# Kernel optimization log

Hardware: AMD Instinct MI355X
Metric: run time of the kernel (lower is better)

Reference implementation:

```python
import jax, jax.numpy as jnp
import numpy as np

H = 64
VOCAB = 64
THRESH_SCALE = 0.4
LN_EPS = 1e-5
NORM_EPS = 1e-12


def setup_inputs() -> dict:
    key = jax.random.key(0)
    ks = jax.random.split(key, 16)
    B, L = 64, 1024
    s = 1.0 / np.sqrt(H)
    inp = {
        "seq": jax.random.randint(ks[0], (B, L), 0, VOCAB),
        "embed_W": jax.random.normal(ks[1], (VOCAB, H), jnp.float32),
        "ff_W1": jax.random.normal(ks[2], (H, 2 * H), jnp.float32) * s,
        "ff_b1": jnp.zeros((2 * H,), jnp.float32),
        "ff_W2": jax.random.normal(ks[3], (2 * H, H), jnp.float32) * s,
        "ff_b2": jnp.zeros((H,), jnp.float32),
        "ln_g": jnp.ones((H,), jnp.float32),
        "ln_b": jnp.zeros((H,), jnp.float32),
        "kp_W": jax.random.normal(ks[4], (H, H), jnp.float32) * s,
        "vp_W": jax.random.normal(ks[5], (H, H), jnp.float32) * s,
        "qp_W": jax.random.normal(ks[6], (H, H), jnp.float32) * s,
        "rp_W": jax.random.normal(ks[7], (H, H), jnp.float32) * s,
        "rp_b": jnp.zeros((H,), jnp.float32),
        "out_W": jax.random.normal(ks[8], (H, VOCAB), jnp.float32) * s,
        "out_b": jnp.zeros((VOCAB,), jnp.float32),
    }
    return inp


def _forward(seq, embed_W, ff_W1, ff_b1, ff_W2, ff_b2, ln_g, ln_b,
             kp_W, vp_W, qp_W, rp_W, rp_b, out_W, out_b):
    h = embed_W[seq]                                    # [B, L, H]
    ff = jnp.maximum(h @ ff_W1 + ff_b1, 0.0) @ ff_W2 + ff_b2
    x = h + ff
    mu = x.mean(-1, keepdims=True)
    var = ((x - mu) ** 2).mean(-1, keepdims=True)       # biased var (torch LayerNorm)
    hn = (x - mu) / jnp.sqrt(var + LN_EPS) * ln_g + ln_b
    B, L, _ = hn.shape

    # Precompute all per-step keys/values, then scan the fast-weight update.
    k_all = hn[:, :-1] @ kp_W                           # [B, L-1, H]
    v_all = hn[:, :-1] @ vp_W                           # [B, L-1, H]
    kn_all = k_all / jnp.maximum(
        jnp.linalg.norm(k_all, axis=-1, keepdims=True), NORM_EPS)

    def step(M, kv):
        kn, v = kv                                      # each [B, H]
        vp = jnp.einsum('bij,bj->bi', M, kn)            # read M along k
        err = jnp.linalg.norm(v - vp, axis=-1)          # [B]
        gate = jnp.where(err > THRESH_SCALE * jnp.linalg.norm(v, axis=-1),
                         1.0, 0.0)                      # hard energy gate
        M = M + gate[:, None, None] * jnp.einsum('bi,bj->bij', v - vp, kn)
        return M, None

    M0 = jnp.zeros((B, H, H), dtype=hn.dtype)
    M, _ = jax.lax.scan(step, M0,
                        (kn_all.transpose(1, 0, 2), v_all.transpose(1, 0, 2)))

    q = hn[:, -1] @ qp_W                                # [B, H]
    r = jnp.einsum('bij,bj->bi', M, q) @ rp_W + rp_b
    return r @ out_W + out_b                            # [B, VOCAB]


def reference(seq, embed_W, ff_W1, ff_b1, ff_W2, ff_b2, ln_g, ln_b,
              kp_W, vp_W, qp_W, rp_W, rp_b, out_W, out_b):
    return _forward(seq, embed_W, ff_W1, ff_b1, ff_W2, ff_b2, ln_g, ln_b,
                    kp_W, vp_W, qp_W, rp_W, rp_b, out_W, out_b)
```

## Files before the change

kernel.cpp:

```cpp
#include <hip/hip_runtime.h>
#include <hip/hip_bf16.h>
#include <math.h>

#define BB 64
#define LL 1024
#define HH 64

typedef float v4f __attribute__((ext_vector_type(4)));
#define F4 __builtin_elementwise_fma

__global__ __launch_bounds__(256, 1)
void token_kernel(const int* __restrict__ seq,
                  const float* __restrict__ embed_W,
                  const float* __restrict__ ff_W1, const float* __restrict__ ff_b1,
                  const float* __restrict__ ff_W2, const float* __restrict__ ff_b2,
                  const float* __restrict__ ln_g, const float* __restrict__ ln_b,
                  const float* __restrict__ kp_W, const float* __restrict__ vp_W,
                  const float* __restrict__ qp_W,
                  float* __restrict__ knv, float* __restrict__ vthr,
                  float* __restrict__ qbuf)
{
    __shared__ __align__(16) float h_s[32][64];
    __shared__ __align__(16) float t1_s[32][128];
    __shared__ __align__(16) float hn_s[32][64];

    const int tid  = threadIdx.x;
    const int tok0 = blockIdx.x * 32;

#pragma unroll
    for (int k = 0; k < 8; ++k) {
        int e   = k * 256 + tid;
        int tok = e >> 6, i = e & 63;
        int s   = seq[tok0 + tok];
        h_s[tok][i] = embed_W[s * 64 + i];
    }
    __syncthreads();

    {
        const int j = tid & 127;
        const int g = tid >> 7;
        float w1c[64];
#pragma unroll
        for (int ii = 0; ii < 64; ++ii) w1c[ii] = ff_W1[ii * 128 + j];
        const float b1j = ff_b1[j];
#pragma unroll
        for (int tk = 0; tk < 16; ++tk) {
            const int tok = g * 16 + tk;
            const float4* h4 = (const float4*)h_s[tok];
            float a0 = b1j, a1 = 0.f, a2 = 0.f, a3 = 0.f;
#pragma unroll
            for (int w = 0; w < 16; ++w) {
                float4 hv = h4[w];
                a0 = fmaf(hv.x, w1c[4*w+0], a0);
                a1 = fmaf(hv.y, w1c[4*w+1], a1);
                a2 = fmaf(hv.z, w1c[4*w+2], a2);
                a3 = fmaf(hv.w, w1c[4*w+3], a3);
            }
            t1_s[tok][j] = fmaxf((a0 + a1) + (a2 + a3), 0.f);
        }
    }
    __syncthreads();

    {
        const int i  = tid & 63;
        const int w4 = tid >> 6;
        const float b2i = ff_b2[i];
        const float gi  = ln_g[i];
        const float bi  = ln_b[i];
        float accf[8];
#pragma unroll
        for (int tk = 0; tk < 8; ++tk) accf[tk] = b2i;
#pragma unroll
        for (int h = 0; h < 2; ++h) {
            float w2c[64];
#pragma unroll
            for (int jj = 0; jj < 64; ++jj) w2c[jj] = ff_W2[(h*64 + jj) * 64 + i];
#pragma unroll
            for (int tk = 0; tk < 8; ++tk) {
                const int tok = w4 * 8 + tk;
                const float4* t4 = (const float4*)&t1_s[tok][h*64];
                float a0 = 0.f, a1 = 0.f, a2 = 0.f, a3 = 0.f;
#pragma unroll
                for (int w = 0; w < 16; ++w) {
                    float4 tv = t4[w];
                    a0 = fmaf(tv.x, w2c[4*w+0], a0);
                    a1 = fmaf(tv.y, w2c[4*w+1], a1);
                    a2 = fmaf(tv.z, w2c[4*w+2], a2);
                    a3 = fmaf(tv.w, w2c[4*w+3], a3);
                }
                accf[tk] += (a0 + a1) + (a2 + a3);
            }
        }
#pragma unroll
        for (int tk = 0; tk < 8; ++tk) {
            const int tok = w4 * 8 + tk;
            float x = h_s[tok][i] + accf[tk];
            float s = x;
#pragma unroll
            for (int m = 32; m > 0; m >>= 1) s += __shfl_xor(s, m);
            float mu = s * (1.f / 64.f);
            float d  = x - mu;
            float s2 = d * d;
#pragma unroll
            for (int m = 32; m > 0; m >>= 1) s2 += __shfl_xor(s2, m);
            float var = s2 * (1.f / 64.f);
            hn_s[tok][i] = d / sqrtf(var + 1e-5f) * gi + bi;
        }
    }
    __syncthreads();

    {
        const int i  = tid & 63;
        const int w4 = tid >> 6;
        float kc[64], vc[64];
#pragma unroll
        for (int ii = 0; ii < 64; ++ii) {
            kc[ii] = kp_W[ii * 64 + i];
            vc[ii] = vp_W[ii * 64 + i];
        }
#pragma unroll
        for (int tk = 0; tk < 8; ++tk) {
            const int tok = w4 * 8 + tk;
            const int tg  = tok0 + tok;
            const int b   = tg >> 10;
            const int t   = tg & 1023;
            const float4* hn4 = (const float4*)hn_s[tok];
            if (t < 1023) {
                float ka0=0.f,ka1=0.f,ka2=0.f,ka3=0.f;
                float va0=0.f,va1=0.f,va2=0.f,va3=0.f;
#pragma unroll
                for (int w = 0; w < 16; ++w) {
                    float4 hv = hn4[w];
                    ka0 = fmaf(hv.x, kc[4*w+0], ka0);
                    ka1 = fmaf(hv.y, kc[4*w+1], ka1);
                    ka2 = fmaf(hv.z, kc[4*w+2], ka2);
                    ka3 = fmaf(hv.w, kc[4*w+3], ka3);
                    va0 = fmaf(hv.x, vc[4*w+0], va0);
                    va1 = fmaf(hv.y, vc[4*w+1], va1);
                    va2 = fmaf(hv.z, vc[4*w+2], va2);
                    va3 = fmaf(hv.w, vc[4*w+3], va3);
                }
                float ka = (ka0 + ka1) + (ka2 + ka3);
                float va = (va0 + va1) + (va2 + va3);
                float kn2 = ka * ka, vn2 = va * va;
#pragma unroll
                for (int m = 32; m > 0; m >>= 1) {
                    kn2 += __shfl_xor(kn2, m);
                    vn2 += __shfl_xor(vn2, m);
                }
                float knorm = fmaxf(sqrtf(kn2), 1e-12f);
                size_t row = ((size_t)b * 1024 + t) * 128;
                knv[row + i]      = ka / knorm;
                knv[row + 64 + i] = va;
                if (i == 0) vthr[b * 1024 + t] = 0.16f * vn2;
            } else {
                float qa0=0.f,qa1=0.f,qa2=0.f,qa3=0.f;
#pragma unroll
                for (int w = 0; w < 16; ++w) {
                    float4 hv = hn4[w];
                    qa0 = fmaf(hv.x, qp_W[(4*w+0)*64 + i], qa0);
                    qa1 = fmaf(hv.y, qp_W[(4*w+1)*64 + i], qa1);
                    qa2 = fmaf(hv.z, qp_W[(4*w+2)*64 + i], qa2);
                    qa3 = fmaf(hv.w, qp_W[(4*w+3)*64 + i], qa3);
                }
                qbuf[b * 64 + i] = (qa0 + qa1) + (qa2 + qa3);
            }
        }
    }
}


template<int CTRL>
__device__ __forceinline__ float dppadd(float x) {
    int y = __builtin_amdgcn_update_dpp(0, __float_as_int(x), CTRL, 0xF, 0xF, true);
    return x + __int_as_float(y);
}

__device__ __forceinline__ float bcast63(float x) {
    return __int_as_float(__builtin_amdgcn_readlane(__float_as_int(x), 63));
}

__device__ __forceinline__ float wave_sum64(float x) {
    x = dppadd<0x111>(x); x = dppadd<0x112>(x);
    x = dppadd<0x114>(x); x = dppadd<0x118>(x);
    x = dppadd<0x142>(x); x = dppadd<0x143>(x);
    return bcast63(x);
}

__device__ __forceinline__ void wsum4(float& a, float& b, float& c, float& d) {
    a = dppadd<0x111>(a); b = dppadd<0x111>(b); c = dppadd<0x111>(c); d = dppadd<0x111>(d);
    a = dppadd<0x112>(a); b = dppadd<0x112>(b); c = dppadd<0x112>(c); d = dppadd<0x112>(d);
    a = dppadd<0x114>(a); b = dppadd<0x114>(b); c = dppadd<0x114>(c); d = dppadd<0x114>(d);
    a = dppadd<0x118>(a); b = dppadd<0x118>(b); c = dppadd<0x118>(c); d = dppadd<0x118>(d);
    a = dppadd<0x142>(a); b = dppadd<0x142>(b); c = dppadd<0x142>(c); d = dppadd<0x142>(d);
    a = dppadd<0x143>(a); b = dppadd<0x143>(b); c = dppadd<0x143>(c); d = dppadd<0x143>(d);
    a = bcast63(a); b = bcast63(b); c = bcast63(c); d = bcast63(d);
}

#define LOADK4(P, ROW) do { \
    const float* r_ = (ROW) + (wid << 4); \
    P##0 = *(const v4f*)(r_ + 0);  P##1 = *(const v4f*)(r_ + 4); \
    P##2 = *(const v4f*)(r_ + 8);  P##3 = *(const v4f*)(r_ + 12); \
} while (0)

#define UPD4(P, G) do { \
    v4f gv_ = {G, G, G, G}; \
    m0 = F4(gv_, P##0, m0); m1 = F4(gv_, P##1, m1); \
    m2 = F4(gv_, P##2, m2); m3 = F4(gv_, P##3, m3); \
} while (0)

#define CHUNK2(UP, UQ, XR, XS, ROW2, ROW3, TH2P, TH3P, PAR) do { \
    UPD4(UP, gdp); \
    UPD4(UQ, gdq); \
    v4f q_ = F4(m0, XR##0, F4(m1, XR##1, F4(m2, XR##2, m3 * XR##3))); \
    float own0_ = (q_.x + q_.y) + (q_.z + q_.w); \
    v4f r_ = F4(m0, XS##0, F4(m1, XS##1, F4(m2, XS##2, m3 * XS##3))); \
    float own1_ = (r_.x + r_.y) + (r_.z + r_.w); \
    ((float2*)pex[PAR][wid])[lane] = make_float2(own0_, own1_); \
    asm volatile("s_waitcnt lgkmcnt(0)\n\ts_barrier" ::: "memory"); \
    float2 p0_ = ((const float2*)pex[PAR][0])[lane]; \
    float2 p1_ = ((const float2*)pex[PAR][1])[lane]; \
    float2 p2_ = ((const float2*)pex[PAR][2])[lane]; \
    float2 p3_ = ((const float2*)pex[PAR][3])[lane]; \
    float knl2_ = (ROW2)[lane]; \
    float knl3_ = (ROW3)[lane]; \
    float vv2_  = (ROW2)[64 + lane]; \
    float vv3_  = (ROW3)[64 + lane]; \
    float th2_  = *(TH2P); \
    float th3_  = *(TH3P); \
    LOADK4(UP, ROW2); \
    LOADK4(UQ, ROW3); \
    float base0_ = (p0_.x + p1_.x) + (p2_.x + p3_.x); \
    float base1_ = (p0_.y + p1_.y) + (p2_.y + p3_.y); \
    float d00_ = vv0 - base0_; \
    float d01_ = vv1 - base1_; \
    float x0_ = d00_ * d00_, x1_ = d00_ * d01_; \
    float x2_ = d01_ * d01_, x3_ = knl2_ * knl3_; \
    wsum4(x0_, x1_, x2_, x3_); \
    bool g0_ = x0_ > th0; \
    float corr_ = fmaf(2.f * c3, x1_, -(c3 * c3) * x0_); \
    float e1_ = g0_ ? (x2_ - corr_) : x2_; \
    bool g1_ = e1_ > th1; \
    float gd0_ = g0_ ? d00_ : 0.f; \
    float d1_  = fmaf(-c3, gd0_, d01_); \
    gdp = gd0_; \
    gdq = g1_ ? d1_ : 0.f; \
    vv0 = vv2_; vv1 = vv3_; th0 = th2_; th1 = th3_; c3 = x3_; \
} while (0)

#define BUF8(CB, NB, TP) \
    CHUNK2(U,V,S,T,(CB)+2*128, (CB)+3*128, (TP)+2, (TP)+3, 0); \
    CHUNK2(S,T,U,V,(CB)+4*128, (CB)+5*128, (TP)+4, (TP)+5, 1); \
    CHUNK2(U,V,S,T,(CB)+6*128, (CB)+7*128, (TP)+6, (TP)+7, 0); \
    CHUNK2(S,T,U,V,(CB)+8*128, (CB)+9*128, (TP)+8, (TP)+9, 1); \
    CHUNK2(U,V,S,T,(CB)+10*128,(CB)+11*128,(TP)+10,(TP)+11,0); \
    CHUNK2(S,T,U,V,(CB)+12*128,(CB)+13*128,(TP)+12,(TP)+13,1); \
    CHUNK2(U,V,S,T,(CB)+14*128,(CB)+15*128,(TP)+14,(TP)+15,0); \
    CHUNK2(S,T,U,V,(NB)+0*128, (NB)+1*128, (TP)+16,(TP)+17,1);

__device__ __forceinline__ void gl2lds_1k(const float* g, float* l, int lane) {
    __builtin_amdgcn_global_load_lds(
        (const __attribute__((address_space(1))) void*)(g + lane * 4),
        (__attribute__((address_space(3))) void*)l, 16, 0, 0);
}

__device__ __forceinline__ void prefetch_quarter(const float* g, float* l,
                                                 int lane, int wid) {
#pragma unroll
    for (int j = 0; j < 2; ++j)
        gl2lds_1k(g + wid * 512 + j * 256, l + wid * 512 + j * 256, lane);
}

__global__ __launch_bounds__(256, 1)
void scan_kernel(const float* __restrict__ knv,
                 const float* __restrict__ vthr,
                 const float* __restrict__ qbuf,
                 const float* __restrict__ rp_W, const float* __restrict__ rp_b,
                 const float* __restrict__ out_W, const float* __restrict__ out_b,
                 float* __restrict__ out)
{
    const int b    = blockIdx.x;
    const int tid  = threadIdx.x;
    const int lane = tid & 63;
    const int wid  = tid >> 6;
    const float* knvb = knv  + (size_t)b * 1024 * 128;
    const float* thrb = vthr + (size_t)b * 1024;

    __shared__ __align__(16) float thr_s[1040];
    __shared__ __align__(16) float buf[3 * 2048];
    __shared__ __align__(16) float pex[2][4][128];
    __shared__ float sh[64];

    v4f m0={0,0,0,0}, m1={0,0,0,0}, m2={0,0,0,0}, m3={0,0,0,0};
    v4f S0,S1,S2,S3;
    v4f T0,T1,T2,T3;
    v4f U0,U1,U2,U3;
    v4f V0,V1,V2,V3;

    if (wid == 0) {
#pragma unroll
        for (int w = 0; w < 4; ++w) gl2lds_1k(thrb + w * 256, thr_s + w * 256, lane);
    }
    prefetch_quarter(knvb,        buf,        lane, wid);
    prefetch_quarter(knvb + 2048, buf + 2048, lane, wid);
    prefetch_quarter(knvb + 4096, buf + 4096, lane, wid);

    {
        float4 z4 = make_float4(0.f, 0.f, 0.f, 0.f);
        ((float4*)pex)[tid] = z4;
    }

    asm volatile("s_waitcnt vmcnt(2) lgkmcnt(0)\n\ts_barrier" ::: "memory");

    LOADK4(S, buf);
    LOADK4(T, buf + 128);
    {
        v4f z_ = {0.f, 0.f, 0.f, 0.f};
        U0=z_;U1=z_;U2=z_;U3=z_;
        V0=z_;V1=z_;V2=z_;V3=z_;
    }
    float vv0 = buf[64 + lane];
    float vv1 = buf[192 + lane];
    float th0 = thr_s[0];
    float th1 = thr_s[1];
    float c3  = wave_sum64(buf[lane] * buf[128 + lane]);
    float gdp = 0.f, gdq = 0.f;

#pragma unroll 1
    for (int c = 0; c < 62; ++c) {
        asm volatile("s_waitcnt vmcnt(2)" ::: "memory");
        const float* cb = buf + (c % 3) * 2048;
        const float* nb = buf + ((c + 1) % 3) * 2048;
        const float* tp = thr_s + c * 16;
        BUF8(cb, nb, tp)
        if (c <= 60)
            prefetch_quarter(knvb + (size_t)(c + 3) * 2048,
                             buf + (c % 3) * 2048, lane, wid);
    }
    asm volatile("s_waitcnt vmcnt(0)" ::: "memory");
    asm volatile("s_barrier" ::: "memory");
    {
        const float* cb = buf + 2 * 2048;
        const float* nb = buf;
        const float* tp = thr_s + 62 * 16;
        BUF8(cb, nb, tp)
    }
    {
        const float* cb = buf;
        const float* nb = buf + 2048;
        const float* tp = thr_s + 63 * 16;
        BUF8(cb, nb, tp)
    }
    UPD4(U, gdp);

    {
        const v4f* qq = (const v4f*)(qbuf + b * 64);
        const int w4i = 4 * wid;
        v4f aq = F4(m0, qq[w4i+0], F4(m1, qq[w4i+1],
                 F4(m2, qq[w4i+2],  m3 * qq[w4i+3])));
        float vq_own = (aq.x + aq.y) + (aq.z + aq.w);
        pex[0][wid][lane] = vq_own;
        asm volatile("s_waitcnt lgkmcnt(0)\n\ts_barrier" ::: "memory");

        if (wid == 0) {
            float vq = (pex[0][0][lane] + pex[0][1][lane])
                     + (pex[0][2][lane] + pex[0][3][lane]);
            sh[lane] = vq;
            asm volatile("s_waitcnt lgkmcnt(0)" ::: "memory");
            float r = rp_b[lane];
#pragma unroll
            for (int ii = 0; ii < 64; ++ii) r = fmaf(sh[ii], rp_W[ii * 64 + lane], r);
            asm volatile("s_waitcnt lgkmcnt(0)" ::: "memory");
            sh[lane] = r;
            asm volatile("s_waitcnt lgkmcnt(0)" ::: "memory");
            float o = out_b[lane];
#pragma unroll
            for (int ii = 0; ii < 64; ++ii) o = fmaf(sh[ii], out_W[ii * 64 + lane], o);
            out[b * 64 + lane] = o;
        }
    }
}

extern "C" void kernel_launch(void* const* d_in, const int* in_sizes, int n_in,
                              void* d_out, int out_size, void* d_ws, size_t ws_size,
                              hipStream_t stream)
{
    const int*   seq   = (const int*)  d_in[0];
    const float* embed = (const float*)d_in[1];
    const float* ffW1  = (const float*)d_in[2];
    const float* ffb1  = (const float*)d_in[3];
    const float* ffW2  = (const float*)d_in[4];
    const float* ffb2  = (const float*)d_in[5];
    const float* lng   = (const float*)d_in[6];
    const float* lnb   = (const float*)d_in[7];
    const float* kpW   = (const float*)d_in[8];
    const float* vpW   = (const float*)d_in[9];
    const float* qpW   = (const float*)d_in[10];
    const float* rpW   = (const float*)d_in[11];
    const float* rpb   = (const float*)d_in[12];
    const float* outW  = (const float*)d_in[13];
    const float* outb  = (const float*)d_in[14];
    float* out = (float*)d_out;

    float* knv  = (float*)d_ws;
    float* vthr = knv  + (size_t)64 * 1024 * 128;
    float* qbuf = vthr + (size_t)64 * 1024;

    token_kernel<<<2048, 256, 0, stream>>>(seq, embed, ffW1, ffb1, ffW2, ffb2,
                                           lng, lnb, kpW, vpW, qpW,
                                           knv, vthr, qbuf);
    scan_kernel<<<64, 256, 0, stream>>>(knv, vthr, qbuf,
                                        rpW, rpb, outW, outb, out);
}
```

Baseline: 366.1 us.

## Process four scan steps per barrier using pairwise key dot-product corrections

The sequential fast-weight scan now handles four timesteps per cross-wave exchange instead of two. It reads M·k for four future keys at once, then applies gated rank-1 corrections using precomputed pairwise key dot products (six wave reductions per stage). This halves the number of block barriers and LDS exchange rounds along the serial dependency chain. In exchange it adds more register pressure (32 v4f key registers), extra DPP reductions and more serial scalar correction math.

Measured after the change: 348.8 us. 4.7% less time.

```diff
diff --git a/kernel.cpp b/kernel.cpp
--- a/kernel.cpp
+++ b/kernel.cpp
@@ -180,21 +180,14 @@
     return __int_as_float(__builtin_amdgcn_readlane(__float_as_int(x), 63));
 }
 
-__device__ __forceinline__ float wave_sum64(float x) {
-    x = dppadd<0x111>(x); x = dppadd<0x112>(x);
-    x = dppadd<0x114>(x); x = dppadd<0x118>(x);
-    x = dppadd<0x142>(x); x = dppadd<0x143>(x);
-    return bcast63(x);
-}
-
-__device__ __forceinline__ void wsum4(float& a, float& b, float& c, float& d) {
-    a = dppadd<0x111>(a); b = dppadd<0x111>(b); c = dppadd<0x111>(c); d = dppadd<0x111>(d);
-    a = dppadd<0x112>(a); b = dppadd<0x112>(b); c = dppadd<0x112>(c); d = dppadd<0x112>(d);
-    a = dppadd<0x114>(a); b = dppadd<0x114>(b); c = dppadd<0x114>(c); d = dppadd<0x114>(d);
-    a = dppadd<0x118>(a); b = dppadd<0x118>(b); c = dppadd<0x118>(c); d = dppadd<0x118>(d);
-    a = dppadd<0x142>(a); b = dppadd<0x142>(b); c = dppadd<0x142>(c); d = dppadd<0x142>(d);
-    a = dppadd<0x143>(a); b = dppadd<0x143>(b); c = dppadd<0x143>(c); d = dppadd<0x143>(d);
-    a = bcast63(a); b = bcast63(b); c = bcast63(c); d = bcast63(d);
+__device__ __forceinline__ void wsum6(float& a, float& b, float& c,
+                                      float& d, float& e, float& f) {
+#define LVL(C) a=dppadd<C>(a); b=dppadd<C>(b); c=dppadd<C>(c); \
+               d=dppadd<C>(d); e=dppadd<C>(e); f=dppadd<C>(f);
+    LVL(0x111) LVL(0x112) LVL(0x114) LVL(0x118) LVL(0x142) LVL(0x143)
+#undef LVL
+    a=bcast63(a); b=bcast63(b); c=bcast63(c);
+    d=bcast63(d); e=bcast63(e); f=bcast63(f);
 }
 
 #define LOADK4(P, ROW) do { \
@@ -209,54 +202,69 @@
     m2 = F4(gv_, P##2, m2); m3 = F4(gv_, P##3, m3); \
 } while (0)
 
-#define CHUNK2(UP, UQ, XR, XS, ROW2, ROW3, TH2P, TH3P, PAR) do { \
-    UPD4(UP, gdp); \
-    UPD4(UQ, gdq); \
-    v4f q_ = F4(m0, XR##0, F4(m1, XR##1, F4(m2, XR##2, m3 * XR##3))); \
-    float own0_ = (q_.x + q_.y) + (q_.z + q_.w); \
-    v4f r_ = F4(m0, XS##0, F4(m1, XS##1, F4(m2, XS##2, m3 * XS##3))); \
-    float own1_ = (r_.x + r_.y) + (r_.z + r_.w); \
-    ((float2*)pex[PAR][wid])[lane] = make_float2(own0_, own1_); \
+#define DOT4(P, OUT) do { \
+    v4f t_ = F4(m0, P##0, F4(m1, P##1, F4(m2, P##2, m3 * P##3))); \
+    OUT = (t_.x + t_.y) + (t_.z + t_.w); \
+} while (0)
+
+#define CHUNK4(U0_, U1_, U2_, U3_, D0_, D1_, D2_, D3_, R4, R5, R6, R7, \
+               T4, T5, T6, T7, PAR) do { \
+    UPD4(U0_, gd0); UPD4(U1_, gd1); UPD4(U2_, gd2); UPD4(U3_, gd3); \
+    float o0_, o1_, o2_, o3_; \
+    DOT4(D0_, o0_); DOT4(D1_, o1_); DOT4(D2_, o2_); DOT4(D3_, o3_); \
+    ((float4*)pex[PAR][wid])[lane] = make_float4(o0_, o1_, o2_, o3_); \
     asm volatile("s_waitcnt lgkmcnt(0)\n\ts_barrier" ::: "memory"); \
-    float2 p0_ = ((const float2*)pex[PAR][0])[lane]; \
-    float2 p1_ = ((const float2*)pex[PAR][1])[lane]; \
-    float2 p2_ = ((const float2*)pex[PAR][2])[lane]; \
-    float2 p3_ = ((const float2*)pex[PAR][3])[lane]; \
-    float knl2_ = (ROW2)[lane]; \
-    float knl3_ = (ROW3)[lane]; \
-    float vv2_  = (ROW2)[64 + lane]; \
-    float vv3_  = (ROW3)[64 + lane]; \
-    float th2_  = *(TH2P); \
-    float th3_  = *(TH3P); \
-    LOADK4(UP, ROW2); \
-    LOADK4(UQ, ROW3); \
-    float base0_ = (p0_.x + p1_.x) + (p2_.x + p3_.x); \
-    float base1_ = (p0_.y + p1_.y) + (p2_.y + p3_.y); \
-    float d00_ = vv0 - base0_; \
-    float d01_ = vv1 - base1_; \
-    float x0_ = d00_ * d00_, x1_ = d00_ * d01_; \
-    float x2_ = d01_ * d01_, x3_ = knl2_ * knl3_; \
-    wsum4(x0_, x1_, x2_, x3_); \
+    float4 p0_ = ((const float4*)pex[PAR][0])[lane]; \
+    float4 p1_ = ((const float4*)pex[PAR][1])[lane]; \
+    float4 p2_ = ((const float4*)pex[PAR][2])[lane]; \
+    float4 p3_ = ((const float4*)pex[PAR][3])[lane]; \
+    float kn4_ = (R4)[lane], kn5_ = (R5)[lane]; \
+    float kn6_ = (R6)[lane], kn7_ = (R7)[lane]; \
+    float vv4_ = (R4)[64 + lane], vv5_ = (R5)[64 + lane]; \
+    float vv6_ = (R6)[64 + lane], vv7_ = (R7)[64 + lane]; \
+    float t4_ = *(T4), t5_ = *(T5), t6_ = *(T6), t7_ = *(T7); \
+    LOADK4(U0_, R4); LOADK4(U1_, R5); LOADK4(U2_, R6); LOADK4(U3_, R7); \
+    float b0_ = (p0_.x + p1_.x) + (p2_.x + p3_.x); \
+    float b1_ = (p0_.y + p1_.y) + (p2_.y + p3_.y); \
+    float b2_ = (p0_.z + p1_.z) + (p2_.z + p3_.z); \
+    float b3_ = (p0_.w + p1_.w) + (p2_.w + p3_.w); \
+    float d0_ = vv0 - b0_, d1_ = vv1 - b1_; \
+    float d2_ = vv2 - b2_, d3_ = vv3 - b3_; \
+    float x0_ = d0_ * d0_, x1_ = d0_ * d1_, x2_ = d1_ * d1_; \
+    float x3_ = kn4_ * kn5_, x4_ = kn4_ * kn6_, x5_ = kn4_ * kn7_; \
+    wsum6(x0_, x1_, x2_, x3_, x4_, x5_); \
     bool g0_ = x0_ > th0; \
-    float corr_ = fmaf(2.f * c3, x1_, -(c3 * c3) * x0_); \
-    float e1_ = g0_ ? (x2_ - corr_) : x2_; \
+    float co1_ = fmaf(2.f * c01, x1_, -(c01 * c01) * x0_); \
+    float e1_ = g0_ ? (x2_ - co1_) : x2_; \
     bool g1_ = e1_ > th1; \
-    float gd0_ = g0_ ? d00_ : 0.f; \
-    float d1_  = fmaf(-c3, gd0_, d01_); \
-    gdp = gd0_; \
-    gdq = g1_ ? d1_ : 0.f; \
-    vv0 = vv2_; vv1 = vv3_; th0 = th2_; th1 = th3_; c3 = x3_; \
+    float gda_ = g0_ ? d0_ : 0.f; \
+    float gdb_ = g1_ ? fmaf(-c01, gda_, d1_) : 0.f; \
+    float d2p_ = fmaf(-c12, gdb_, fmaf(-c02, gda_, d2_)); \
+    float d3p_ = fmaf(-c13, gdb_, fmaf(-c03, gda_, d3_)); \
+    float y0_ = d2p_ * d2p_, y1_ = d2p_ * d3p_, y2_ = d3p_ * d3p_; \
+    float y3_ = kn5_ * kn6_, y4_ = kn5_ * kn7_, y5_ = kn6_ * kn7_; \
+    wsum6(y0_, y1_, y2_, y3_, y4_, y5_); \
+    bool g2_ = y0_ > th2; \
+    float co2_ = fmaf(2.f * c23, y1_, -(c23 * c23) * y0_); \
+    float e3_ = g2_ ? (y2_ - co2_) : y2_; \
+    bool g3_ = e3_ > th3; \
+    float gdc_ = g2_ ? d2p_ : 0.f; \
+    float gdd_ = g3_ ? fmaf(-c23, gdc_, d3p_) : 0.f; \
+    gd0 = gda_; gd1 = gdb_; gd2 = gdc_; gd3 = gdd_; \
+    c01 = x3_; c02 = x4_; c03 = x5_; c12 = y3_; c13 = y4_; c23 = y5_; \
+    vv0 = vv4_; vv1 = vv5_; vv2 = vv6_; vv3 = vv7_; \
+    th0 = t4_; th1 = t5_; th2 = t6_; th3 = t7_; \
 } while (0)
 
-#define BUF8(CB, NB, TP) \
-    CHUNK2(U,V,S,T,(CB)+2*128, (CB)+3*128, (TP)+2, (TP)+3, 0); \
-    CHUNK2(S,T,U,V,(CB)+4*128, (CB)+5*128, (TP)+4, (TP)+5, 1); \
-    CHUNK2(U,V,S,T,(CB)+6*128, (CB)+7*128, (TP)+6, (TP)+7, 0); \
-    CHUNK2(S,T,U,V,(CB)+8*128, (CB)+9*128, (TP)+8, (TP)+9, 1); \
-    CHUNK2(U,V,S,T,(CB)+10*128,(CB)+11*128,(TP)+10,(TP)+11,0); \
-    CHUNK2(S,T,U,V,(CB)+12*128,(CB)+13*128,(TP)+12,(TP)+13,1); \
-    CHUNK2(U,V,S,T,(CB)+14*128,(CB)+15*128,(TP)+14,(TP)+15,0); \
-    CHUNK2(S,T,U,V,(NB)+0*128, (NB)+1*128, (TP)+16,(TP)+17,1);
+#define BUF4(CB, NB, TP) \
+    CHUNK4(B0,B1,B2,B3, A0,A1,A2,A3, (CB)+4*128,(CB)+5*128,(CB)+6*128,(CB)+7*128, \
+           (TP)+4,(TP)+5,(TP)+6,(TP)+7, 0); \
+    CHUNK4(A0,A1,A2,A3, B0,B1,B2,B3, (CB)+8*128,(CB)+9*128,(CB)+10*128,(CB)+11*128, \
+           (TP)+8,(TP)+9,(TP)+10,(TP)+11, 1); \
+    CHUNK4(B0,B1,B2,B3, A0,A1,A2,A3, (CB)+12*128,(CB)+13*128,(CB)+14*128,(CB)+15*128, \
+           (TP)+12,(TP)+13,(TP)+14,(TP)+15, 0); \
+    CHUNK4(A0,A1,A2,A3, B0,B1,B2,B3, (NB)+0*128,(NB)+1*128,(NB)+2*128,(NB)+3*128, \
+           (TP)+16,(TP)+17,(TP)+18,(TP)+19, 1);
 
 __device__ __forceinline__ void gl2lds_1k(const float* g, float* l, int lane) {
     __builtin_amdgcn_global_load_lds(
@@ -288,14 +296,12 @@
 
     __shared__ __align__(16) float thr_s[1040];
     __shared__ __align__(16) float buf[3 * 2048];
-    __shared__ __align__(16) float pex[2][4][128];
+    __shared__ __align__(16) float pex[2][4][256];
     __shared__ float sh[64];
 
     v4f m0={0,0,0,0}, m1={0,0,0,0}, m2={0,0,0,0}, m3={0,0,0,0};
-    v4f S0,S1,S2,S3;
-    v4f T0,T1,T2,T3;
-    v4f U0,U1,U2,U3;
-    v4f V0,V1,V2,V3;
+    v4f A00,A01,A02,A03, A10,A11,A12,A13, A20,A21,A22,A23, A30,A31,A32,A33;
+    v4f B00,B01,B02,B03, B10,B11,B12,B13, B20,B21,B22,B23, B30,B31,B32,B33;
 
     if (wid == 0) {
 #pragma unroll
@@ -305,26 +311,27 @@
     prefetch_quarter(knvb + 2048, buf + 2048, lane, wid);
     prefetch_quarter(knvb + 4096, buf + 4096, lane, wid);
 
-    {
-        float4 z4 = make_float4(0.f, 0.f, 0.f, 0.f);
-        ((float4*)pex)[tid] = z4;
-    }
-
     asm volatile("s_waitcnt vmcnt(2) lgkmcnt(0)\n\ts_barrier" ::: "memory");
 
-    LOADK4(S, buf);
-    LOADK4(T, buf + 128);
+    LOADK4(A0, buf + 0*128); LOADK4(A1, buf + 1*128);
+    LOADK4(A2, buf + 2*128); LOADK4(A3, buf + 3*128);
     {
         v4f z_ = {0.f, 0.f, 0.f, 0.f};
-        U0=z_;U1=z_;U2=z_;U3=z_;
-        V0=z_;V1=z_;V2=z_;V3=z_;
-    }
-    float vv0 = buf[64 + lane];
-    float vv1 = buf[192 + lane];
-    float th0 = thr_s[0];
-    float th1 = thr_s[1];
-    float c3  = wave_sum64(buf[lane] * buf[128 + lane]);
-    float gdp = 0.f, gdq = 0.f;
+        B00=z_;B01=z_;B02=z_;B03=z_; B10=z_;B11=z_;B12=z_;B13=z_;
+        B20=z_;B21=z_;B22=z_;B23=z_; B30=z_;B31=z_;B32=z_;B33=z_;
+    }
+    float vv0 = buf[0*128+64+lane], vv1 = buf[1*128+64+lane];
+    float vv2 = buf[2*128+64+lane], vv3 = buf[3*128+64+lane];
+    float th0 = thr_s[0], th1 = thr_s[1], th2 = thr_s[2], th3 = thr_s[3];
+    float c01, c02, c03, c12, c13, c23;
+    {
+        float k0_ = buf[0*128+lane], k1_ = buf[1*128+lane];
+        float k2_ = buf[2*128+lane], k3_ = buf[3*128+lane];
+        c01 = k0_*k1_; c02 = k0_*k2_; c03 = k0_*k3_;
+        c12 = k1_*k2_; c13 = k1_*k3_; c23 = k2_*k3_;
+        wsum6(c01, c02, c03, c12, c13, c23);
+    }
+    float gd0 = 0.f, gd1 = 0.f, gd2 = 0.f, gd3 = 0.f;
 
 #pragma unroll 1
     for (int c = 0; c < 62; ++c) {
@@ -332,7 +339,7 @@
         const float* cb = buf + (c % 3) * 2048;
         const float* nb = buf + ((c + 1) % 3) * 2048;
         const float* tp = thr_s + c * 16;
-        BUF8(cb, nb, tp)
+        BUF4(cb, nb, tp)
         if (c <= 60)
             prefetch_quarter(knvb + (size_t)(c + 3) * 2048,
                              buf + (c % 3) * 2048, lane, wid);
@@ -343,15 +350,15 @@
         const float* cb = buf + 2 * 2048;
         const float* nb = buf;
         const float* tp = thr_s + 62 * 16;
-        BUF8(cb, nb, tp)
+        BUF4(cb, nb, tp)
     }
     {
         const float* cb = buf;
         const float* nb = buf + 2048;
         const float* tp = thr_s + 63 * 16;
-        BUF8(cb, nb, tp)
-    }
-    UPD4(U, gdp);
+        BUF4(cb, nb, tp)
+    }
+    UPD4(B0, gd0); UPD4(B1, gd1); UPD4(B2, gd2);
 
     {
         const v4f* qq = (const v4f*)(qbuf + b * 64);
```

## Register-tile token_kernel matmuls to reuse shared-memory activation loads

Applied to the files above, without the earlier changes.

Restructures the FF1, FF2 and K/V projection matmuls in token_kernel into register tiles. Each thread now computes 2 output columns by 4–8 tokens and streams weight rows in chunks of 4, replacing the old scheme of caching a full 64-entry weight column per thread. Each float4 read of activations from shared memory is reused across more FMAs, and the large per-thread weight arrays go away. Cost is extra syncs and a staging pass of FF and K/V results through shared memory before LayerNorm and normalization. The scan kernel, which likely dominates total time, is unchanged.

After: 374.7 us. 1.02x slower.

```diff
diff --git a/kernel.cpp b/kernel.cpp
--- a/kernel.cpp
+++ b/kernel.cpp
@@ -37,26 +37,95 @@
     __syncthreads();
 
     {
-        const int j = tid & 127;
-        const int g = tid >> 7;
-        float w1c[64];
-#pragma unroll
-        for (int ii = 0; ii < 64; ++ii) w1c[ii] = ff_W1[ii * 128 + j];
-        const float b1j = ff_b1[j];
-#pragma unroll
-        for (int tk = 0; tk < 16; ++tk) {
-            const int tok = g * 16 + tk;
-            const float4* h4 = (const float4*)h_s[tok];
-            float a0 = b1j, a1 = 0.f, a2 = 0.f, a3 = 0.f;
-#pragma unroll
-            for (int w = 0; w < 16; ++w) {
-                float4 hv = h4[w];
-                a0 = fmaf(hv.x, w1c[4*w+0], a0);
-                a1 = fmaf(hv.y, w1c[4*w+1], a1);
-                a2 = fmaf(hv.z, w1c[4*w+2], a2);
-                a3 = fmaf(hv.w, w1c[4*w+3], a3);
-            }
-            t1_s[tok][j] = fmaxf((a0 + a1) + (a2 + a3), 0.f);
+        const int jj = tid & 63;
+        const int tg = tid >> 6;
+        float a[2][8][4];
+        const float b10 = ff_b1[jj];
+        const float b11 = ff_b1[jj + 64];
+#pragma unroll
+        for (int t = 0; t < 8; ++t) {
+            a[0][t][0] = b10; a[0][t][1] = 0.f; a[0][t][2] = 0.f; a[0][t][3] = 0.f;
+            a[1][t][0] = b11; a[1][t][1] = 0.f; a[1][t][2] = 0.f; a[1][t][3] = 0.f;
+        }
+#pragma unroll
+        for (int cc = 0; cc < 16; ++cc) {
+            float w0[4], w1[4];
+#pragma unroll
+            for (int r = 0; r < 4; ++r) {
+                w0[r] = ff_W1[(4*cc + r) * 128 + jj];
+                w1[r] = ff_W1[(4*cc + r) * 128 + jj + 64];
+            }
+#pragma unroll
+            for (int t = 0; t < 8; ++t) {
+                const float4 hv = ((const float4*)h_s[tg * 8 + t])[cc];
+                a[0][t][0] = fmaf(hv.x, w0[0], a[0][t][0]);
+                a[0][t][1] = fmaf(hv.y, w0[1], a[0][t][1]);
+                a[0][t][2] = fmaf(hv.z, w0[2], a[0][t][2]);
+                a[0][t][3] = fmaf(hv.w, w0[3], a[0][t][3]);
+                a[1][t][0] = fmaf(hv.x, w1[0], a[1][t][0]);
+                a[1][t][1] = fmaf(hv.y, w1[1], a[1][t][1]);
+                a[1][t][2] = fmaf(hv.z, w1[2], a[1][t][2]);
+                a[1][t][3] = fmaf(hv.w, w1[3], a[1][t][3]);
+            }
+        }
+#pragma unroll
+        for (int t = 0; t < 8; ++t) {
+            const int tok = tg * 8 + t;
+            t1_s[tok][jj]      = fmaxf((a[0][t][0] + a[0][t][1])
+                                     + (a[0][t][2] + a[0][t][3]), 0.f);
+            t1_s[tok][jj + 64] = fmaxf((a[1][t][0] + a[1][t][1])
+                                     + (a[1][t][2] + a[1][t][3]), 0.f);
+        }
+    }
+    __syncthreads();
+
+    {
+        const int ii = tid & 31;
+        const int tg = tid >> 5;
+        const int i0 = ii, i1 = ii + 32;
+        float accf[2][4];
+        const float b20 = ff_b2[i0], b21 = ff_b2[i1];
+#pragma unroll
+        for (int t = 0; t < 4; ++t) { accf[0][t] = b20; accf[1][t] = b21; }
+#pragma unroll
+        for (int h = 0; h < 2; ++h) {
+            float a[2][4][4];
+#pragma unroll
+            for (int t = 0; t < 4; ++t)
+#pragma unroll
+                for (int r = 0; r < 4; ++r) { a[0][t][r] = 0.f; a[1][t][r] = 0.f; }
+#pragma unroll
+            for (int cc = 0; cc < 16; ++cc) {
+                float w0[4], w1[4];
+#pragma unroll
+                for (int r = 0; r < 4; ++r) {
+                    w0[r] = ff_W2[(h*64 + 4*cc + r) * 64 + i0];
+                    w1[r] = ff_W2[(h*64 + 4*cc + r) * 64 + i1];
+                }
+#pragma unroll
+                for (int t = 0; t < 4; ++t) {
+                    const float4 tv = ((const float4*)&t1_s[tg * 4 + t][h * 64])[cc];
+                    a[0][t][0] = fmaf(tv.x, w0[0], a[0][t][0]);
+                    a[0][t][1] = fmaf(tv.y, w0[1], a[0][t][1]);
+                    a[0][t][2] = fmaf(tv.z, w0[2], a[0][t][2]);
+                    a[0][t][3] = fmaf(tv.w, w0[3], a[0][t][3]);
+                    a[1][t][0] = fmaf(tv.x, w1[0], a[1][t][0]);
+                    a[1][t][1] = fmaf(tv.y, w1[1], a[1][t][1]);
+                    a[1][t][2] = fmaf(tv.z, w1[2], a[1][t][2]);
+                    a[1][t][3] = fmaf(tv.w, w1[3], a[1][t][3]);
+                }
+            }
+#pragma unroll
+            for (int t = 0; t < 4; ++t) {
+                accf[0][t] += (a[0][t][0] + a[0][t][1]) + (a[0][t][2] + a[0][t][3]);
+                accf[1][t] += (a[1][t][0] + a[1][t][1]) + (a[1][t][2] + a[1][t][3]);
+            }
+        }
+#pragma unroll
+        for (int t = 0; t < 4; ++t) {
+            const int tok = tg * 4 + t;
+            hn_s[tok][i0] = h_s[tok][i0] + accf[0][t];
+            hn_s[tok][i1] = h_s[tok][i1] + accf[1][t];
         }
     }
     __syncthreads();
@@ -64,37 +133,12 @@
     {
         const int i  = tid & 63;
         const int w4 = tid >> 6;
-        const float b2i = ff_b2[i];
-        const float gi  = ln_g[i];
-        const float bi  = ln_b[i];
-        float accf[8];
-#pragma unroll
-        for (int tk = 0; tk < 8; ++tk) accf[tk] = b2i;
-#pragma unroll
-        for (int h = 0; h < 2; ++h) {
-            float w2c[64];
-#pragma unroll
-            for (int jj = 0; jj < 64; ++jj) w2c[jj] = ff_W2[(h*64 + jj) * 64 + i];
-#pragma unroll
-            for (int tk = 0; tk < 8; ++tk) {
-                const int tok = w4 * 8 + tk;
-                const float4* t4 = (const float4*)&t1_s[tok][h*64];
-                float a0 = 0.f, a1 = 0.f, a2 = 0.f, a3 = 0.f;
-#pragma unroll
-                for (int w = 0; w < 16; ++w) {
-                    float4 tv = t4[w];
-                    a0 = fmaf(tv.x, w2c[4*w+0], a0);
-                    a1 = fmaf(tv.y, w2c[4*w+1], a1);
-                    a2 = fmaf(tv.z, w2c[4*w+2], a2);
-                    a3 = fmaf(tv.w, w2c[4*w+3], a3);
-                }
-                accf[tk] += (a0 + a1) + (a2 + a3);
-            }
-        }
+        const float gi = ln_g[i];
+        const float bi = ln_b[i];
 #pragma unroll
         for (int tk = 0; tk < 8; ++tk) {
             const int tok = w4 * 8 + tk;
-            float x = h_s[tok][i] + accf[tk];
+            float x = hn_s[tok][i];
             float s = x;
 #pragma unroll
             for (int m = 32; m > 0; m >>= 1) s += __shfl_xor(s, m);
@@ -110,38 +154,71 @@
     __syncthreads();
 
     {
+        const int ii = tid & 31;
+        const int tg = tid >> 5;
+        const int i0 = ii, i1 = ii + 32;
+        float ak[2][4][4], av[2][4][4];
+#pragma unroll
+        for (int t = 0; t < 4; ++t)
+#pragma unroll
+            for (int r = 0; r < 4; ++r) {
+                ak[0][t][r] = 0.f; ak[1][t][r] = 0.f;
+                av[0][t][r] = 0.f; av[1][t][r] = 0.f;
+            }
+#pragma unroll
+        for (int cc = 0; cc < 16; ++cc) {
+            float wk0[4], wk1[4], wv0[4], wv1[4];
+#pragma unroll
+            for (int r = 0; r < 4; ++r) {
+                wk0[r] = kp_W[(4*cc + r) * 64 + i0];
+                wk1[r] = kp_W[(4*cc + r) * 64 + i1];
+                wv0[r] = vp_W[(4*cc + r) * 64 + i0];
+                wv1[r] = vp_W[(4*cc + r) * 64 + i1];
+            }
+#pragma unroll
+            for (int t = 0; t < 4; ++t) {
+                const float4 hv = ((const float4*)hn_s[tg * 4 + t])[cc];
+                ak[0][t][0] = fmaf(hv.x, wk0[0], ak[0][t][0]);
+                ak[0][t][1] = fmaf(hv.y, wk0[1], ak[0][t][1]);
+                ak[0][t][2] = fmaf(hv.z, wk0[2], ak[0][t][2]);
+                ak[0][t][3] = fmaf(hv.w, wk0[3], ak[0][t][3]);
+                ak[1][t][0] = fmaf(hv.x, wk1[0], ak[1][t][0]);
+                ak[1][t][1] = fmaf(hv.y, wk1[1], ak[1][t][1]);
+                ak[1][t][2] = fmaf(hv.z, wk1[2], ak[1][t][2]);
+                ak[1][t][3] = fmaf(hv.w, wk1[3], ak[1][t][3]);
+                av[0][t][0] = fmaf(hv.x, wv0[0], av[0][t][0]);
+                av[0][t][1] = fmaf(hv.y, wv0[1], av[0][t][1]);
+                av[0][t][2] = fmaf(hv.z, wv0[2], av[0][t][2]);
+                av[0][t][3] = fmaf(hv.w, wv0[3], av[0][t][3]);
+                av[1][t][0] = fmaf(hv.x, wv1[0], av[1][t][0]);
+                av[1][t][1] = fmaf(hv.y, wv1[1], av[1][t][1]);
+                av[1][t][2] = fmaf(hv.z, wv1[2], av[1][t][2]);
+                av[1][t][3] = fmaf(hv.w, wv1[3], av[1][t][3]);
+            }
+        }
+#pragma unroll
+        for (int t = 0; t < 4; ++t) {
+            const int tok = tg * 4 + t;
+            t1_s[tok][i0]      = (ak[0][t][0] + ak[0][t][1]) + (ak[0][t][2] + ak[0][t][3]);
+            t1_s[tok][i1]      = (ak[1][t][0] + ak[1][t][1]) + (ak[1][t][2] + ak[1][t][3]);
+            t1_s[tok][64 + i0] = (av[0][t][0] + av[0][t][1]) + (av[0][t][2] + av[0][t][3]);
+            t1_s[tok][64 + i1] = (av[1][t][0] + av[1][t][1]) + (av[1][t][2] + av[1][t][3]);
+        }
+    }
+    __syncthreads();
+
+    {
         const int i  = tid & 63;
         const int w4 = tid >> 6;
-        float kc[64], vc[64];
-#pragma unroll
-        for (int ii = 0; ii < 64; ++ii) {
-            kc[ii] = kp_W[ii * 64 + i];
-            vc[ii] = vp_W[ii * 64 + i];
-        }
 #pragma unroll
         for (int tk = 0; tk < 8; ++tk) {
             const int tok = w4 * 8 + tk;
-            const int tg  = tok0 + tok;
-            const int b   = tg >> 10;
-            const int t   = tg & 1023;
-            const float4* hn4 = (const float4*)hn_s[tok];
+            const int tg_ = tok0 + tok;
+            const int b   = tg_ >> 10;
+            const int t   = tg_ & 1023;
             if (t < 1023) {
-                float ka0=0.f,ka1=0.f,ka2=0.f,ka3=0.f;
-                float va0=0.f,va1=0.f,va2=0.f,va3=0.f;
-#pragma unroll
-                for (int w = 0; w < 16; ++w) {
-                    float4 hv = hn4[w];
-                    ka0 = fmaf(hv.x, kc[4*w+0], ka0);
-                    ka1 = fmaf(hv.y, kc[4*w+1], ka1);
-                    ka2 = fmaf(hv.z, kc[4*w+2], ka2);
-                    ka3 = fmaf(hv.w, kc[4*w+3], ka3);
-                    va0 = fmaf(hv.x, vc[4*w+0], va0);
-                    va1 = fmaf(hv.y, vc[4*w+1], va1);
-                    va2 = fmaf(hv.z, vc[4*w+2], va2);
-                    va3 = fmaf(hv.w, vc[4*w+3], va3);
-                }
-                float ka = (ka0 + ka1) + (ka2 + ka3);
-                float va = (va0 + va1) + (va2 + va3);
+                float ka = t1_s[tok][i];
+                float va = t1_s[tok][64 + i];
                 float kn2 = ka * ka, vn2 = va * va;
 #pragma unroll
                 for (int m = 32; m > 0; m >>= 1) {
@@ -154,6 +231,7 @@
                 knv[row + 64 + i] = va;
                 if (i == 0) vthr[b * 1024 + t] = 0.16f * vn2;
             } else {
+                const float4* hn4 = (const float4*)hn_s[tok];
                 float qa0=0.f,qa1=0.f,qa2=0.f,qa3=0.f;
 #pragma unroll
                 for (int w = 0; w < 16; ++w) {
```

## Software-pipeline scan readout one step ahead using Gram-matrix corrections

Applied to the files above, without the earlier changes.

Restructures the sequential fast-weight scan so each step computes the M·k readout for the next pair before the pending rank-1 update is applied. The missing contribution is added back through precomputed key dot products (Ga/Gb terms). The cross-wave exchange barrier now sits at the end of the step, so it overlaps with the next step's loads and updates and shortens the serial dependency chain. In exchange, each step adds more DPP reductions (8 instead of 4) and extra FMAs, and the corrected readout may differ slightly in floating-point results from the direct form.

Result: slower. 395.7 us (+8.1%).

```diff
diff --git a/kernel.cpp b/kernel.cpp
--- a/kernel.cpp
+++ b/kernel.cpp
@@ -187,14 +187,14 @@
     return bcast63(x);
 }
 
-__device__ __forceinline__ void wsum4(float& a, float& b, float& c, float& d) {
-    a = dppadd<0x111>(a); b = dppadd<0x111>(b); c = dppadd<0x111>(c); d = dppadd<0x111>(d);
-    a = dppadd<0x112>(a); b = dppadd<0x112>(b); c = dppadd<0x112>(c); d = dppadd<0x112>(d);
-    a = dppadd<0x114>(a); b = dppadd<0x114>(b); c = dppadd<0x114>(c); d = dppadd<0x114>(d);
-    a = dppadd<0x118>(a); b = dppadd<0x118>(b); c = dppadd<0x118>(c); d = dppadd<0x118>(d);
-    a = dppadd<0x142>(a); b = dppadd<0x142>(b); c = dppadd<0x142>(c); d = dppadd<0x142>(d);
-    a = dppadd<0x143>(a); b = dppadd<0x143>(b); c = dppadd<0x143>(c); d = dppadd<0x143>(d);
-    a = bcast63(a); b = bcast63(b); c = bcast63(c); d = bcast63(d);
+__device__ __forceinline__ void wsum8(float& a, float& b, float& c, float& d,
+                                      float& e, float& f, float& g, float& h) {
+#define LVL(C) a=dppadd<C>(a); b=dppadd<C>(b); c=dppadd<C>(c); d=dppadd<C>(d); \
+               e=dppadd<C>(e); f=dppadd<C>(f); g=dppadd<C>(g); h=dppadd<C>(h);
+    LVL(0x111) LVL(0x112) LVL(0x114) LVL(0x118) LVL(0x142) LVL(0x143)
+#undef LVL
+    a=bcast63(a); b=bcast63(b); c=bcast63(c); d=bcast63(d);
+    e=bcast63(e); f=bcast63(f); g=bcast63(g); h=bcast63(h);
 }
 
 #define LOADK4(P, ROW) do { \
@@ -209,54 +209,58 @@
     m2 = F4(gv_, P##2, m2); m3 = F4(gv_, P##3, m3); \
 } while (0)
 
-#define CHUNK2(UP, UQ, XR, XS, ROW2, ROW3, TH2P, TH3P, PAR) do { \
-    UPD4(UP, gdp); \
-    UPD4(UQ, gdq); \
-    v4f q_ = F4(m0, XR##0, F4(m1, XR##1, F4(m2, XR##2, m3 * XR##3))); \
-    float own0_ = (q_.x + q_.y) + (q_.z + q_.w); \
-    v4f r_ = F4(m0, XS##0, F4(m1, XS##1, F4(m2, XS##2, m3 * XS##3))); \
-    float own1_ = (r_.x + r_.y) + (r_.z + r_.w); \
-    ((float2*)pex[PAR][wid])[lane] = make_float2(own0_, own1_); \
-    asm volatile("s_waitcnt lgkmcnt(0)\n\ts_barrier" ::: "memory"); \
-    float2 p0_ = ((const float2*)pex[PAR][0])[lane]; \
-    float2 p1_ = ((const float2*)pex[PAR][1])[lane]; \
-    float2 p2_ = ((const float2*)pex[PAR][2])[lane]; \
-    float2 p3_ = ((const float2*)pex[PAR][3])[lane]; \
+#define CHUNK2L(P0_, P1_, ROW2, ROW3, TH2P, TH3P, PAR) do { \
+    float2 p0_ = ((const float2*)pex[(PAR)^1][0])[lane]; \
+    float2 p1_ = ((const float2*)pex[(PAR)^1][1])[lane]; \
+    float2 p2_ = ((const float2*)pex[(PAR)^1][2])[lane]; \
+    float2 p3_ = ((const float2*)pex[(PAR)^1][3])[lane]; \
+    UPD4(P0_, gdp); \
+    UPD4(P1_, gdq); \
+    LOADK4(P0_, ROW2); \
+    LOADK4(P1_, ROW3); \
     float knl2_ = (ROW2)[lane]; \
     float knl3_ = (ROW3)[lane]; \
     float vv2_  = (ROW2)[64 + lane]; \
     float vv3_  = (ROW3)[64 + lane]; \
     float th2_  = *(TH2P); \
     float th3_  = *(TH3P); \
-    LOADK4(UP, ROW2); \
-    LOADK4(UQ, ROW3); \
     float base0_ = (p0_.x + p1_.x) + (p2_.x + p3_.x); \
     float base1_ = (p0_.y + p1_.y) + (p2_.y + p3_.y); \
-    float d00_ = vv0 - base0_; \
-    float d01_ = vv1 - base1_; \
-    float x0_ = d00_ * d00_, x1_ = d00_ * d01_; \
-    float x2_ = d01_ * d01_, x3_ = knl2_ * knl3_; \
-    wsum4(x0_, x1_, x2_, x3_); \
+    float vp0_ = fmaf(Gb0, gdq, fmaf(Ga0, gdp, base0_)); \
+    float vp1_ = fmaf(Gb1, gdq, fmaf(Ga1, gdp, base1_)); \
+    float d00_ = vv0 - vp0_; \
+    float d01_ = vv1 - vp1_; \
+    float x0_ = d00_ * d00_, x1_ = d00_ * d01_, x2_ = d01_ * d01_; \
+    float y0_ = knl0 * knl2_, y1_ = knl1 * knl2_; \
+    float y2_ = knl0 * knl3_, y3_ = knl1 * knl3_, y4_ = knl2_ * knl3_; \
+    wsum8(x0_, x1_, x2_, y0_, y1_, y2_, y3_, y4_); \
     bool g0_ = x0_ > th0; \
-    float corr_ = fmaf(2.f * c3, x1_, -(c3 * c3) * x0_); \
+    float corr_ = fmaf(2.f * c01, x1_, -(c01 * c01) * x0_); \
     float e1_ = g0_ ? (x2_ - corr_) : x2_; \
     bool g1_ = e1_ > th1; \
     float gd0_ = g0_ ? d00_ : 0.f; \
-    float d1_  = fmaf(-c3, gd0_, d01_); \
+    float d1_  = fmaf(-c01, gd0_, d01_); \
     gdp = gd0_; \
     gdq = g1_ ? d1_ : 0.f; \
-    vv0 = vv2_; vv1 = vv3_; th0 = th2_; th1 = th3_; c3 = x3_; \
+    v4f q_ = F4(m0, P0_##0, F4(m1, P0_##1, F4(m2, P0_##2, m3 * P0_##3))); \
+    float own0_ = (q_.x + q_.y) + (q_.z + q_.w); \
+    v4f r_ = F4(m0, P1_##0, F4(m1, P1_##1, F4(m2, P1_##2, m3 * P1_##3))); \
+    float own1_ = (r_.x + r_.y) + (r_.z + r_.w); \
+    ((float2*)pex[PAR][wid])[lane] = make_float2(own0_, own1_); \
+    knl0 = knl2_; knl1 = knl3_; vv0 = vv2_; vv1 = vv3_; th0 = th2_; th1 = th3_; \
+    Ga0 = y0_; Gb0 = y1_; Ga1 = y2_; Gb1 = y3_; c01 = y4_; \
+    asm volatile("s_waitcnt lgkmcnt(0)\n\ts_barrier" ::: "memory"); \
 } while (0)
 
-#define BUF8(CB, NB, TP) \
-    CHUNK2(U,V,S,T,(CB)+2*128, (CB)+3*128, (TP)+2, (TP)+3, 0); \
-    CHUNK2(S,T,U,V,(CB)+4*128, (CB)+5*128, (TP)+4, (TP)+5, 1); \
-    CHUNK2(U,V,S,T,(CB)+6*128, (CB)+7*128, (TP)+6, (TP)+7, 0); \
-    CHUNK2(S,T,U,V,(CB)+8*128, (CB)+9*128, (TP)+8, (TP)+9, 1); \
-    CHUNK2(U,V,S,T,(CB)+10*128,(CB)+11*128,(TP)+10,(TP)+11,0); \
-    CHUNK2(S,T,U,V,(CB)+12*128,(CB)+13*128,(TP)+12,(TP)+13,1); \
-    CHUNK2(U,V,S,T,(CB)+14*128,(CB)+15*128,(TP)+14,(TP)+15,0); \
-    CHUNK2(S,T,U,V,(NB)+0*128, (NB)+1*128, (TP)+16,(TP)+17,1);
+#define BUF8L(CB, NB, TP) \
+    CHUNK2L(U,V,(CB)+2*128, (CB)+3*128, (TP)+2, (TP)+3, 0); \
+    CHUNK2L(S,T,(CB)+4*128, (CB)+5*128, (TP)+4, (TP)+5, 1); \
+    CHUNK2L(U,V,(CB)+6*128, (CB)+7*128, (TP)+6, (TP)+7, 0); \
+    CHUNK2L(S,T,(CB)+8*128, (CB)+9*128, (TP)+8, (TP)+9, 1); \
+    CHUNK2L(U,V,(CB)+10*128,(CB)+11*128,(TP)+10,(TP)+11,0); \
+    CHUNK2L(S,T,(CB)+12*128,(CB)+13*128,(TP)+12,(TP)+13,1); \
+    CHUNK2L(U,V,(CB)+14*128,(CB)+15*128,(TP)+14,(TP)+15,0); \
+    CHUNK2L(S,T,(NB)+0*128, (NB)+1*128, (TP)+16,(TP)+17,1);
 
 __device__ __forceinline__ void gl2lds_1k(const float* g, float* l, int lane) {
     __builtin_amdgcn_global_load_lds(
@@ -319,11 +323,14 @@
         U0=z_;U1=z_;U2=z_;U3=z_;
         V0=z_;V1=z_;V2=z_;V3=z_;
     }
-    float vv0 = buf[64 + lane];
-    float vv1 = buf[192 + lane];
-    float th0 = thr_s[0];
-    float th1 = thr_s[1];
-    float c3  = wave_sum64(buf[lane] * buf[128 + lane]);
+    float knl0 = buf[lane];
+    float knl1 = buf[128 + lane];
+    float vv0  = buf[64 + lane];
+    float vv1  = buf[192 + lane];
+    float th0  = thr_s[0];
+    float th1  = thr_s[1];
+    float c01  = wave_sum64(knl0 * knl1);
+    float Ga0 = 0.f, Gb0 = 0.f, Ga1 = 0.f, Gb1 = 0.f;
     float gdp = 0.f, gdq = 0.f;
 
 #pragma unroll 1
@@ -332,7 +339,7 @@
         const float* cb = buf + (c % 3) * 2048;
         const float* nb = buf + ((c + 1) % 3) * 2048;
         const float* tp = thr_s + c * 16;
-        BUF8(cb, nb, tp)
+        BUF8L(cb, nb, tp)
         if (c <= 60)
             prefetch_quarter(knvb + (size_t)(c + 3) * 2048,
                              buf + (c % 3) * 2048, lane, wid);
@@ -343,13 +350,13 @@
         const float* cb = buf + 2 * 2048;
         const float* nb = buf;
         const float* tp = thr_s + 62 * 16;
-        BUF8(cb, nb, tp)
+        BUF8L(cb, nb, tp)
     }
     {
         const float* cb = buf;
         const float* nb = buf + 2048;
         const float* tp = thr_s + 63 * 16;
-        BUF8(cb, nb, tp)
+        BUF8L(cb, nb, tp)
     }
     UPD4(U, gdp);
 
```
